# Performance work log

Hardware: AMD Instinct MI355X
Metric: run time of the kernel (lower is better)

The kernel has to match this reference:

```python
import jax, jax.numpy as jnp
import numpy as np

B, T, W, L, H, TW = 2, 4096, 2048, 2048, 8, 4
HD = L // H  # head dim for block-diagonal gate projections


def setup_inputs() -> dict:
    key = jax.random.key(0)
    ks = jax.random.split(key, 16)
    inv_sqrt_w = 1.0 / np.sqrt(W)
    inv_sqrt_l = 1.0 / np.sqrt(L)
    inv_sqrt_hd = 1.0 / np.sqrt(HD)
    return {
        "x": jax.random.normal(ks[0], (B, T, W), dtype=jnp.float32),
        "segment_pos": jnp.tile(jnp.arange(T, dtype=jnp.int32), (B, 1)),
        # linear_y, linear_x: width -> lru_width
        "w_y": jax.random.normal(ks[1], (W, L), dtype=jnp.float32) * inv_sqrt_w,
        "b_y": jnp.zeros((L,), dtype=jnp.float32),
        "w_x": jax.random.normal(ks[2], (W, L), dtype=jnp.float32) * inv_sqrt_w,
        "b_x": jnp.zeros((L,), dtype=jnp.float32),
        # linear_out: lru_width -> width
        "w_out": jax.random.normal(ks[3], (L, W), dtype=jnp.float32) * inv_sqrt_l,
        "b_out": jnp.zeros((W,), dtype=jnp.float32),
        # depthwise causal temporal conv, kernel [TW, L]
        "conv_w": jax.random.normal(ks[4], (TW, L), dtype=jnp.float32) / np.sqrt(TW),
        "conv_b": jnp.zeros((L,), dtype=jnp.float32),
        # RG-LRU: a_param and two block-diagonal gate projections
        "a_param": jax.random.uniform(ks[5], (L,), dtype=jnp.float32, minval=-2.0, maxval=1.0),
        "igate_w": jax.random.normal(ks[6], (H, HD, HD), dtype=jnp.float32) * inv_sqrt_hd,
        "igate_b": jnp.zeros((H, HD), dtype=jnp.float32),
        "agate_w": jax.random.normal(ks[7], (H, HD, HD), dtype=jnp.float32) * inv_sqrt_hd,
        "agate_b": jnp.zeros((H, HD), dtype=jnp.float32),
    }


def _block_diag_linear(u, w, b):
    # u: [B,T,L] -> [B,T,H,HD] blockwise projected -> [B,T,L]
    uh = u.reshape(u.shape[0], u.shape[1], H, HD)
    y = jnp.einsum("bthd,hde->bthe", uh, w) + b
    return y.reshape(u.shape)


def _forward(x, segment_pos, w_y, b_y, w_x, b_x, w_out, b_out,
             conv_w, conv_b, a_param, igate_w, igate_b, agate_w, agate_b):
    # gate branch: linear_y + tanh-approx GELU
    y = jax.nn.gelu(jnp.einsum("btw,wl->btl", x, w_y) + b_y, approximate=True)
    # recurrent branch: linear_x
    xb = jnp.einsum("btw,wl->btl", x, w_x) + b_x
    # causal depthwise temporal conv (width TW), zero history before t=0
    x_pad = jnp.pad(xb, ((0, 0), (TW - 1, 0), (0, 0)))
    conv = conv_b + sum(conv_w[j] * x_pad[:, j:j + T] for j in range(TW))
    # RG-LRU gates
    gate_x = jax.nn.sigmoid(_block_diag_linear(conv, igate_w, igate_b))
    gate_a = jax.nn.sigmoid(_block_diag_linear(conv, agate_w, agate_b))
    log_a = -8.0 * gate_a * jax.nn.softplus(a_param)  # [B,T,L]
    a = jnp.exp(log_a)
    reset = (segment_pos == 0)[..., None]  # [B,T,1]
    multiplier = jnp.sqrt(1.0 - jnp.exp(2.0 * log_a))
    multiplier = jnp.where(reset, 1.0, multiplier)
    normed = conv * gate_x * multiplier
    a_masked = jnp.where(reset, 0.0, a)
    # diagonal linear recurrence: h_t = a_t * h_{t-1} + normed_t
    def step(h, inp):
        a_t, x_t = inp
        h = a_t * h + x_t
        return h, h
    h0 = jnp.zeros((x.shape[0], L), dtype=x.dtype)
    _, hs = jax.lax.scan(step, h0, (a_masked.transpose(1, 0, 2), normed.transpose(1, 0, 2)))
    hs = hs.transpose(1, 0, 2)  # [B,T,L]
    # elementwise gate then output projection
    return jnp.einsum("btl,lw->btw", hs * y, w_out) + b_out


def reference(x, segment_pos, w_y, b_y, w_x, b_x, w_out, b_out,
              conv_w, conv_b, a_param, igate_w, igate_b, agate_w, agate_b):
    return _forward(x, segment_pos, w_y, b_y, w_x, b_x, w_out, b_out,
                    conv_w, conv_b, a_param, igate_w, igate_b, agate_w, agate_b)
```

## Files before the change

kernel.cpp:

```cpp
#include <hip/hip_runtime.h>
#include <cstdint>
#include <math.h>

typedef _Float16 f16;
typedef f16 f16x8 __attribute__((ext_vector_type(8)));
typedef f16 f16x4 __attribute__((ext_vector_type(4)));
typedef float f32x4 __attribute__((ext_vector_type(4)));

#define BATCH 2
#define TSEQ 4096
#define WID 2048
#define LRU 2048
#define NHEAD 8
#define HDIM 256
#define MTOT (BATCH * TSEQ)
#define CT 128
#define NC (TSEQ / CT)

__device__ __forceinline__ void gl2lds16(const f16* g, f16* l) {
  __builtin_amdgcn_global_load_lds(
      (__attribute__((address_space(1))) uint32_t*)(uintptr_t)g,
      (__attribute__((address_space(3))) uint32_t*)(uint32_t)(uintptr_t)l,
      16, 0, 0);
}

__device__ __forceinline__ float sigmoidf_(float x) { return 1.f / (1.f + expf(-x)); }
__device__ __forceinline__ float f16bits_to_f(uint32_t b) {
  return (float)__builtin_bit_cast(f16, (uint16_t)b);
}

__global__ void cast_f32_f16_kernel(const float* __restrict__ in, f16* __restrict__ out, int n4) {
  int i = blockIdx.x * 256 + threadIdx.x;
  if (i >= n4) return;
  float4 v = ((const float4*)in)[i];
  f16x4 o = { (f16)v.x, (f16)v.y, (f16)v.z, (f16)v.w };
  ((f16x4*)out)[i] = o;
}

__global__ void transpose_big_kernel(const float* __restrict__ s0, const float* __restrict__ s1,
                                     const float* __restrict__ s2, f16* __restrict__ d0,
                                     f16* __restrict__ d1, f16* __restrict__ d2) {
  __shared__ float tile[32][33];
  const int R = 2048, C = 2048;
  const float* ib = blockIdx.z == 0 ? s0 : (blockIdx.z == 1 ? s1 : s2);
  f16* ob = blockIdx.z == 0 ? d0 : (blockIdx.z == 1 ? d1 : d2);
  int c0 = blockIdx.x * 32, r0 = blockIdx.y * 32;
  int tx = threadIdx.x, ty = threadIdx.y;
#pragma unroll
  for (int i = 0; i < 32; i += 8)
    tile[ty + i][tx] = ib[(long long)(r0 + ty + i) * C + c0 + tx];
  __syncthreads();
#pragma unroll
  for (int i = 0; i < 32; i += 8)
    ob[(long long)(c0 + ty + i) * R + r0 + tx] = (f16)tile[tx][ty + i];
}

__global__ void transpose_small_kernel(const float* __restrict__ ig, const float* __restrict__ ag,
                                       f16* __restrict__ igT, f16* __restrict__ agT) {
  __shared__ float tile[32][33];
  int z = blockIdx.z;
  const float* ib = (z < 8 ? ig : ag) + (long long)(z & 7) * HDIM * HDIM;
  f16* ob = (z < 8 ? igT : agT) + (long long)(z & 7) * HDIM * HDIM;
  int c0 = blockIdx.x * 32, r0 = blockIdx.y * 32;
  int tx = threadIdx.x, ty = threadIdx.y;
#pragma unroll
  for (int i = 0; i < 32; i += 8)
    tile[ty + i][tx] = ib[(r0 + ty + i) * HDIM + c0 + tx];
  __syncthreads();
#pragma unroll
  for (int i = 0; i < 32; i += 8)
    ob[(c0 + ty + i) * HDIM + r0 + tx] = (f16)tile[tx][ty + i];
}

__global__ __launch_bounds__(256, 2) void gemm_dual(
    const f16* __restrict__ A, const f16* __restrict__ B1T, const f16* __restrict__ B2T,
    const float* __restrict__ b1, const float* __restrict__ b2,
    f16* __restrict__ Y, f16* __restrict__ X2, int M, int N, int K) {
  __shared__ __align__(16) f16 As[128 * 32];
  __shared__ __align__(16) f16 B1s[128 * 32];
  __shared__ __align__(16) f16 B2s[128 * 32];
  const int m0 = blockIdx.x * 128, n0 = blockIdx.y * 128;
  const int t = threadIdx.x;
  const int lane = t & 63, wave = t >> 6;
  const int wr = (wave >> 1) * 64, wc = (wave & 1) * 64;
  const int l15 = lane & 15, quad = lane >> 4;
  const int srow = t >> 2, scol = (t & 3) * 8;

  const f16* Ag = A + (long long)(m0 + srow) * K + scol;
  const f16* B1g = B1T + (long long)(n0 + srow) * K + scol;
  const f16* B2g = B2T + (long long)(n0 + srow) * K + scol;

  f32x4 c1[4][4] = {};
  f32x4 c2[4][4] = {};
  for (int k0 = 0; k0 < K; k0 += 32) {
    gl2lds16(Ag, &As[t * 8]);   gl2lds16(Ag + (long long)64 * K, &As[64 * 32 + t * 8]);
    gl2lds16(B1g, &B1s[t * 8]); gl2lds16(B1g + (long long)64 * K, &B1s[64 * 32 + t * 8]);
    gl2lds16(B2g, &B2s[t * 8]); gl2lds16(B2g + (long long)64 * K, &B2s[64 * 32 + t * 8]);
    Ag += 32; B1g += 32; B2g += 32;
    __syncthreads();
    f16x8 af[4], b1f[4], b2f[4];
#pragma unroll
    for (int i = 0; i < 4; ++i)
      af[i] = *(const f16x8*)&As[(wr + i * 16 + l15) * 32 + quad * 8];
#pragma unroll
    for (int j = 0; j < 4; ++j) {
      b1f[j] = *(const f16x8*)&B1s[(wc + j * 16 + l15) * 32 + quad * 8];
      b2f[j] = *(const f16x8*)&B2s[(wc + j * 16 + l15) * 32 + quad * 8];
    }
#pragma unroll
    for (int i = 0; i < 4; ++i)
#pragma unroll
      for (int j = 0; j < 4; ++j) {
        c1[i][j] = __builtin_amdgcn_mfma_f32_16x16x32_f16(af[i], b1f[j], c1[i][j], 0, 0, 0);
        c2[i][j] = __builtin_amdgcn_mfma_f32_16x16x32_f16(af[i], b2f[j], c2[i][j], 0, 0, 0);
      }
    __syncthreads();
  }
#pragma unroll
  for (int i = 0; i < 4; ++i) {
#pragma unroll
    for (int j = 0; j < 4; ++j) {
      const int col = n0 + wc + j * 16 + l15;
      const float b1v = b1[col], b2v = b2[col];
      const int row0 = m0 + wr + i * 16 + quad * 4;
#pragma unroll
      for (int r = 0; r < 4; ++r) {
        long long off = (long long)(row0 + r) * N + col;
        float v = c1[i][j][r] + b1v;
        float u = v + 0.044715f * v * v * v;
        float g = 0.5f * v * (1.f + tanhf(0.7978845608028654f * u));
        Y[off] = (f16)g;
        X2[off] = (f16)(c2[i][j][r] + b2v);
      }
    }
  }
}

__global__ __launch_bounds__(256, 2) void gemm_bt(
    const f16* __restrict__ A, const f16* __restrict__ BT, const float* __restrict__ bias,
    float* __restrict__ Cf, int M, int N, int K) {
  __shared__ __align__(16) f16 As[128 * 32];
  __shared__ __align__(16) f16 Bs[128 * 32];
  const int m0 = blockIdx.x * 128, n0 = blockIdx.y * 128;
  const int t = threadIdx.x;
  const int lane = t & 63, wave = t >> 6;
  const int wr = (wave >> 1) * 64, wc = (wave & 1) * 64;
  const int l15 = lane & 15, quad = lane >> 4;
  const int srow = t >> 2, scol = (t & 3) * 8;

  const f16* Ag = A + (long long)(m0 + srow) * K + scol;
  const f16* Bg = BT + (long long)(n0 + srow) * K + scol;

  f32x4 acc[4][4] = {};
  for (int k0 = 0; k0 < K; k0 += 32) {
    gl2lds16(Ag, &As[t * 8]); gl2lds16(Ag + (long long)64 * K, &As[64 * 32 + t * 8]);
    gl2lds16(Bg, &Bs[t * 8]); gl2lds16(Bg + (long long)64 * K, &Bs[64 * 32 + t * 8]);
    Ag += 32; Bg += 32;
    __syncthreads();
    f16x8 af[4], bf[4];
#pragma unroll
    for (int i = 0; i < 4; ++i)
      af[i] = *(const f16x8*)&As[(wr + i * 16 + l15) * 32 + quad * 8];
#pragma unroll
    for (int j = 0; j < 4; ++j)
      bf[j] = *(const f16x8*)&Bs[(wc + j * 16 + l15) * 32 + quad * 8];
#pragma unroll
    for (int i = 0; i < 4; ++i)
#pragma unroll
      for (int j = 0; j < 4; ++j)
        acc[i][j] = __builtin_amdgcn_mfma_f32_16x16x32_f16(af[i], bf[j], acc[i][j], 0, 0, 0);
    __syncthreads();
  }
#pragma unroll
  for (int i = 0; i < 4; ++i) {
#pragma unroll
    for (int j = 0; j < 4; ++j) {
      const int col = n0 + wc + j * 16 + l15;
      const float bv = bias[col];
      const int row0 = m0 + wr + i * 16 + quad * 4;
#pragma unroll
      for (int r = 0; r < 4; ++r)
        Cf[(long long)(row0 + r) * N + col] = acc[i][j][r] + bv;
    }
  }
}

__global__ __launch_bounds__(256, 2) void gates_fused(
    const f16* __restrict__ XBh, const float* __restrict__ cw, const float* __restrict__ cb,
    const f16* __restrict__ BiT, const f16* __restrict__ BaT,
    const float* __restrict__ ib, const float* __restrict__ ab,
    const float* __restrict__ a_param, const int* __restrict__ segpos,
    uint32_t* __restrict__ AN, float* __restrict__ Ac, float* __restrict__ Hc) {
  __shared__ __align__(16) f16 As[128 * 256];
  __shared__ __align__(16) f16 Bi[128 * 32];
  __shared__ __align__(16) f16 Ba[128 * 32];
  const int m0 = blockIdx.x * 128;
  const int h = blockIdx.y >> 1;
  const int half = blockIdx.y & 1;
  const int ncol0 = h * HDIM + half * 128;
  const int t = threadIdx.x;
  const int lane = t & 63, wave = t >> 6;
  const int wr = (wave >> 1) * 64, wc = (wave & 1) * 64;
  const int l15 = lane & 15, quad = lane >> 4;

#pragma unroll 4
  for (int it = 0; it < 16; ++it) {
    int idx = it * 256 + t;
    int r = idx >> 5, kc = idx & 31;
    int m = m0 + r, tpos = m & (TSEQ - 1);
    int colbase = h * HDIM + kc * 8;
    float acc[8];
    {
      float4 c0 = *(const float4*)&cb[colbase];
      float4 c1 = *(const float4*)&cb[colbase + 4];
      acc[0] = c0.x; acc[1] = c0.y; acc[2] = c0.z; acc[3] = c0.w;
      acc[4] = c1.x; acc[5] = c1.y; acc[6] = c1.z; acc[7] = c1.w;
    }
#pragma unroll
    for (int d = 0; d < 4; ++d) {
      if (tpos >= d) {
        f16x8 xv = *(const f16x8*)&XBh[(long long)(m - d) * LRU + colbase];
        float4 w0 = *(const float4*)&cw[(3 - d) * LRU + colbase];
        float4 w1 = *(const float4*)&cw[(3 - d) * LRU + colbase + 4];
        acc[0] += w0.x * (float)xv[0]; acc[1] += w0.y * (float)xv[1];
        acc[2] += w0.z * (float)xv[2]; acc[3] += w0.w * (float)xv[3];
        acc[4] += w1.x * (float)xv[4]; acc[5] += w1.y * (float)xv[5];
        acc[6] += w1.z * (float)xv[6]; acc[7] += w1.w * (float)xv[7];
      }
    }
    f16x8 o;
#pragma unroll
    for (int k = 0; k < 8; ++k) o[k] = (f16)acc[k];
    int gs = (kc & ~7) | ((kc ^ r) & 7);
    *(f16x8*)&As[r * 256 + gs * 8] = o;
  }
  __syncthreads();

  const int srow = t >> 2, scol = (t & 3) * 8;
  const f16* Big = BiT + (long long)(ncol0 + srow) * HDIM + scol;
  const f16* Bag = BaT + (long long)(ncol0 + srow) * HDIM + scol;
  f32x4 ci[4][4] = {};
  f32x4 ca[4][4] = {};
  for (int k0 = 0; k0 < HDIM; k0 += 32) {
    gl2lds16(Big, &Bi[t * 8]); gl2lds16(Big + 64 * HDIM, &Bi[64 * 32 + t * 8]);
    gl2lds16(Bag, &Ba[t * 8]); gl2lds16(Bag + 64 * HDIM, &Ba[64 * 32 + t * 8]);
    Big += 32; Bag += 32;
    __syncthreads();
    f16x8 af[4], bif[4], baf[4];
#pragma unroll
    for (int i = 0; i < 4; ++i) {
      int row = wr + i * 16 + l15;
      int g = (k0 >> 3) + quad;
      int gsw = (g & ~7) | ((g ^ row) & 7);
      af[i] = *(const f16x8*)&As[row * 256 + gsw * 8];
    }
#pragma unroll
    for (int j = 0; j < 4; ++j) {
      bif[j] = *(const f16x8*)&Bi[(wc + j * 16 + l15) * 32 + quad * 8];
      baf[j] = *(const f16x8*)&Ba[(wc + j * 16 + l15) * 32 + quad * 8];
    }
#pragma unroll
    for (int i = 0; i < 4; ++i)
#pragma unroll
      for (int j = 0; j < 4; ++j) {
        ci[i][j] = __builtin_amdgcn_mfma_f32_16x16x32_f16(af[i], bif[j], ci[i][j], 0, 0, 0);
        ca[i][j] = __builtin_amdgcn_mfma_f32_16x16x32_f16(af[i], baf[j], ca[i][j], 0, 0, 0);
      }
    __syncthreads();
  }

  const int mb = m0 >> 12;
  const int cch = (m0 & (TSEQ - 1)) >> 7;
  float Aw[4], hw[4];
#pragma unroll
  for (int j = 0; j < 4; ++j) {
    const int cl = wc + j * 16 + l15;
    const int col = ncol0 + cl;
    const float ibv = ib[col], abv = ab[col];
    const float sp = log1pf(expf(a_param[col]));
    float A4[4], h4[4];
#pragma unroll
    for (int i = 0; i < 4; ++i) {
      float Aseg = 1.f, hseg = 0.f;
#pragma unroll
      for (int r = 0; r < 4; ++r) {
        const int rowL = wr + i * 16 + quad * 4 + r;
        const int row = m0 + rowL;
        float gx = sigmoidf_(ci[i][j][r] + ibv);
        float ga = sigmoidf_(ca[i][j][r] + abv);
        float la = -8.f * ga * sp;
        bool rs = (segpos[row] == 0);
        float a = rs ? 0.f : expf(la);
        uint32_t afx = __float2uint_rn(a * 65536.f);
        if (afx > 65535u) afx = 65535u;
        float aq = (float)afx * (1.f / 65536.f);
        int cfull = half * 128 + cl;
        int g = cfull >> 3, e = cfull & 7;
        int gsw = (g & ~7) | ((g ^ rowL) & 7);
        float cv = (float)As[rowL * 256 + gsw * 8 + e];
        float mult = rs ? 1.f : sqrtf(fmaxf(1.f - aq * aq, 0.f));
        f16 nh = (f16)(cv * gx * mult);
        AN[(long long)row * LRU + col] =
            afx | ((uint32_t)__builtin_bit_cast(uint16_t, nh) << 16);
        float xq = (float)nh;
        hseg = aq * hseg + xq;
        Aseg *= aq;
      }
      A4[i] = Aseg; h4[i] = hseg;
    }
#pragma unroll
    for (int i = 0; i < 4; ++i) {
      float A = A4[i], hv = h4[i];
#pragma unroll
      for (int d = 1; d <= 2; d <<= 1) {
        int src = quad >= d ? lane - 16 * d : lane;
        float Ap = __shfl(A, src);
        float hp = __shfl(hv, src);
        if (quad >= d) { hv = A * hp + hv; A = Ap * A; }
      }
      A4[i] = __shfl(A, 48 + l15);
      h4[i] = __shfl(hv, 48 + l15);
    }
    float Awv = 1.f, hwv = 0.f;
#pragma unroll
    for (int i = 0; i < 4; ++i) { hwv = A4[i] * hwv + h4[i]; Awv *= A4[i]; }
    Aw[j] = Awv; hw[j] = hwv;
  }
  float* carry = (float*)Bi;
  __syncthreads();
  if (wr == 0 && quad == 0) {
#pragma unroll
    for (int j = 0; j < 4; ++j) {
      int cl = wc + j * 16 + l15;
      carry[cl * 2] = Aw[j]; carry[cl * 2 + 1] = hw[j];
    }
  }
  __syncthreads();
  if (wr == 64 && quad == 0) {
#pragma unroll
    for (int j = 0; j < 4; ++j) {
      int cl = wc + j * 16 + l15;
      float At = carry[cl * 2], ht = carry[cl * 2 + 1];
      float A = At * Aw[j];
      float hv = Aw[j] * ht + hw[j];
      int o = (mb * NC + cch) * LRU + ncol0 + cl;
      Ac[o] = A; Hc[o] = hv;
    }
  }
}

__global__ void scan2_kernel(const float* __restrict__ Ac, const float* __restrict__ Hc,
                             float* __restrict__ P) {
  int l = blockIdx.x * 256 + threadIdx.x;
  int b = blockIdx.y;
  float hv = 0.f;
#pragma unroll 8
  for (int c = 0; c < NC; ++c) {
    int o = (b * NC + c) * LRU + l;
    P[o] = hv;
    hv = Ac[o] * hv + Hc[o];
  }
}

__global__ void scan3_kernel(const uint32_t* __restrict__ AN,
                             const float* __restrict__ P, const f16* __restrict__ Yh,
                             f16* __restrict__ G) {
  int l = blockIdx.x * 256 + threadIdx.x;
  int c = blockIdx.y, b = blockIdx.z;
  long long base = ((long long)b * TSEQ + (long long)c * CT) * LRU + l;
  float hv = P[(b * NC + c) * LRU + l];
#pragma unroll 4
  for (int s = 0; s < CT; ++s) {
    long long o = base + (long long)s * LRU;
    uint32_t p = AN[o];
    float a = (float)(p & 0xFFFFu) * (1.f / 65536.f);
    float x = f16bits_to_f(p >> 16);
    hv = a * hv + x;
    G[o] = (f16)(hv * (float)Yh[o]);
  }
}

extern "C" void kernel_launch(void* const* d_in, const int* in_sizes, int n_in,
                              void* d_out, int out_size, void* d_ws, size_t ws_size,
                              hipStream_t stream) {
  (void)in_sizes; (void)n_in; (void)out_size; (void)ws_size;
  const float* x          = (const float*)d_in[0];
  const int*   segment_pos= (const int*)d_in[1];
  const float* w_y        = (const float*)d_in[2];
  const float* b_y        = (const float*)d_in[3];
  const float* w_x        = (const float*)d_in[4];
  const float* b_x        = (const float*)d_in[5];
  const float* w_out      = (const float*)d_in[6];
  const float* b_out      = (const float*)d_in[7];
  const float* conv_w     = (const float*)d_in[8];
  const float* conv_b     = (const float*)d_in[9];
  const float* a_param    = (const float*)d_in[10];
  const float* igate_w    = (const float*)d_in[11];
  const float* igate_b    = (const float*)d_in[12];
  const float* agate_w    = (const float*)d_in[13];
  const float* agate_b    = (const float*)d_in[14];
  float* out = (float*)d_out;

  char* base = (char*)d_ws;
  size_t off = 0;
  auto alloc = [&](size_t nbytes) -> void* {
    void* p = base + off;
    off = (off + nbytes + 255) & ~(size_t)255;
    return p;
  };
  f16*     Xh    = (f16*)alloc((size_t)MTOT * LRU * 2);
  f16*     Yh    = (f16*)alloc((size_t)MTOT * LRU * 2);
  f16*     XBh   = (f16*)alloc((size_t)MTOT * LRU * 2);
  uint32_t* AN   = (uint32_t*)alloc((size_t)MTOT * LRU * 4);
  f16*     wyT   = (f16*)alloc((size_t)WID * LRU * 2);
  f16*     wxT   = (f16*)alloc((size_t)WID * LRU * 2);
  f16*     woutT = (f16*)alloc((size_t)LRU * WID * 2);
  f16*     igwT  = (f16*)alloc((size_t)NHEAD * HDIM * HDIM * 2);
  f16*     agwT  = (f16*)alloc((size_t)NHEAD * HDIM * HDIM * 2);
  float*   Ac    = (float*)alloc((size_t)BATCH * NC * LRU * 4);
  float*   Hc    = (float*)alloc((size_t)BATCH * NC * LRU * 4);
  float*   Pc    = (float*)alloc((size_t)BATCH * NC * LRU * 4);
  f16*     G     = Xh;

  dim3 tb32(32, 8);
  cast_f32_f16_kernel<<<(MTOT * LRU / 4 + 255) / 256, 256, 0, stream>>>(x, Xh, MTOT * LRU / 4);
  transpose_big_kernel<<<dim3(64, 64, 3), tb32, 0, stream>>>(w_y, w_x, w_out, wyT, wxT, woutT);
  transpose_small_kernel<<<dim3(8, 8, 16), tb32, 0, stream>>>(igate_w, agate_w, igwT, agwT);
  gemm_dual<<<dim3(MTOT / 128, LRU / 128), 256, 0, stream>>>(
      Xh, wyT, wxT, b_y, b_x, Yh, XBh, MTOT, LRU, WID);
  gates_fused<<<dim3(MTOT / 128, 2 * NHEAD), 256, 0, stream>>>(
      XBh, conv_w, conv_b, igwT, agwT, igate_b, agate_b, a_param, segment_pos, AN, Ac, Hc);
  scan2_kernel<<<dim3(LRU / 256, BATCH), 256, 0, stream>>>(Ac, Hc, Pc);
  scan3_kernel<<<dim3(LRU / 256, NC, BATCH), 256, 0, stream>>>(AN, Pc, Yh, G);
  gemm_bt<<<dim3(MTOT / 128, WID / 128), 256, 0, stream>>>(G, woutT, b_out, out, MTOT, WID, LRU);
}
```

Measured before the change: 573.2 us.

## Fuse chunked scan into gates kernel with decoupled look-back carry chain

Replaces the gates kernel plus two separate scan kernels with a single kernel that computes the full within-tile scan in registers. Carries pass between sequential chunks through global flags and atomics, with block order set by a ticket counter, so the packed AN intermediate (a 32-bit value per element written and re-read) is no longer needed. The conv stage now reuses a register window of XBh rows instead of reloading four rows per output, and the cast/transpose prep kernels are merged into one launch. In exchange, chunks along time are serialized through spin-waits on flags.

```diff
diff --git a/kernel.cpp b/kernel.cpp
--- a/kernel.cpp
+++ b/kernel.cpp
@@ -14,8 +14,8 @@
 #define NHEAD 8
 #define HDIM 256
 #define MTOT (BATCH * TSEQ)
-#define CT 128
-#define NC (TSEQ / CT)
+#define NCHUNK 32
+#define NMT 64
 
 __device__ __forceinline__ void gl2lds16(const f16* g, f16* l) {
   __builtin_amdgcn_global_load_lds(
@@ -25,27 +25,39 @@
 }
 
 __device__ __forceinline__ float sigmoidf_(float x) { return 1.f / (1.f + expf(-x)); }
-__device__ __forceinline__ float f16bits_to_f(uint32_t b) {
-  return (float)__builtin_bit_cast(f16, (uint16_t)b);
-}
-
-__global__ void cast_f32_f16_kernel(const float* __restrict__ in, f16* __restrict__ out, int n4) {
-  int i = blockIdx.x * 256 + threadIdx.x;
-  if (i >= n4) return;
-  float4 v = ((const float4*)in)[i];
-  f16x4 o = { (f16)v.x, (f16)v.y, (f16)v.z, (f16)v.w };
-  ((f16x4*)out)[i] = o;
-}
-
-__global__ void transpose_big_kernel(const float* __restrict__ s0, const float* __restrict__ s1,
-                                     const float* __restrict__ s2, f16* __restrict__ d0,
-                                     f16* __restrict__ d1, f16* __restrict__ d2) {
+
+__global__ void prep_kernel(const float* __restrict__ x, f16* __restrict__ Xh,
+                            const float* __restrict__ w_y, const float* __restrict__ w_x,
+                            const float* __restrict__ w_out,
+                            f16* __restrict__ wyT, f16* __restrict__ wxT, f16* __restrict__ woutT,
+                            const float* __restrict__ ig, const float* __restrict__ ag,
+                            f16* __restrict__ igT, f16* __restrict__ agT) {
   __shared__ float tile[32][33];
-  const int R = 2048, C = 2048;
-  const float* ib = blockIdx.z == 0 ? s0 : (blockIdx.z == 1 ? s1 : s2);
-  f16* ob = blockIdx.z == 0 ? d0 : (blockIdx.z == 1 ? d1 : d2);
-  int c0 = blockIdx.x * 32, r0 = blockIdx.y * 32;
-  int tx = threadIdx.x, ty = threadIdx.y;
+  const int bid = blockIdx.x, t = threadIdx.x;
+  if (bid < 16384) {
+    int i = bid * 256 + t;
+    float4 v = ((const float4*)x)[i];
+    f16x4 o = { (f16)v.x, (f16)v.y, (f16)v.z, (f16)v.w };
+    ((f16x4*)Xh)[i] = o;
+    return;
+  }
+  const int tx = t & 31, ty = t >> 5;
+  const float* ib; f16* ob; int R, C, c0, r0;
+  if (bid < 28672) {
+    int idx = bid - 16384;
+    int z = idx >> 12, tl = idx & 4095;
+    ib = z == 0 ? w_y : (z == 1 ? w_x : w_out);
+    ob = z == 0 ? wyT : (z == 1 ? wxT : woutT);
+    R = 2048; C = 2048;
+    c0 = (tl & 63) * 32; r0 = (tl >> 6) * 32;
+  } else {
+    int idx = bid - 28672;
+    int z = idx >> 6, tl = idx & 63;
+    ib = (z < 8 ? ig : ag) + (long long)(z & 7) * HDIM * HDIM;
+    ob = (z < 8 ? igT : agT) + (long long)(z & 7) * HDIM * HDIM;
+    R = HDIM; C = HDIM;
+    c0 = (tl & 7) * 32; r0 = (tl >> 3) * 32;
+  }
 #pragma unroll
   for (int i = 0; i < 32; i += 8)
     tile[ty + i][tx] = ib[(long long)(r0 + ty + i) * C + c0 + tx];
@@ -53,23 +65,6 @@
 #pragma unroll
   for (int i = 0; i < 32; i += 8)
     ob[(long long)(c0 + ty + i) * R + r0 + tx] = (f16)tile[tx][ty + i];
-}
-
-__global__ void transpose_small_kernel(const float* __restrict__ ig, const float* __restrict__ ag,
-                                       f16* __restrict__ igT, f16* __restrict__ agT) {
-  __shared__ float tile[32][33];
-  int z = blockIdx.z;
-  const float* ib = (z < 8 ? ig : ag) + (long long)(z & 7) * HDIM * HDIM;
-  f16* ob = (z < 8 ? igT : agT) + (long long)(z & 7) * HDIM * HDIM;
-  int c0 = blockIdx.x * 32, r0 = blockIdx.y * 32;
-  int tx = threadIdx.x, ty = threadIdx.y;
-#pragma unroll
-  for (int i = 0; i < 32; i += 8)
-    tile[ty + i][tx] = ib[(r0 + ty + i) * HDIM + c0 + tx];
-  __syncthreads();
-#pragma unroll
-  for (int i = 0; i < 32; i += 8)
-    ob[(c0 + ty + i) * HDIM + r0 + tx] = (f16)tile[tx][ty + i];
 }
 
 __global__ __launch_bounds__(256, 2) void gemm_dual(
@@ -185,54 +180,75 @@
   }
 }
 
-__global__ __launch_bounds__(256, 2) void gates_fused(
+__global__ __launch_bounds__(256, 2) void gates_scan(
     const f16* __restrict__ XBh, const float* __restrict__ cw, const float* __restrict__ cb,
     const f16* __restrict__ BiT, const f16* __restrict__ BaT,
     const float* __restrict__ ib, const float* __restrict__ ab,
     const float* __restrict__ a_param, const int* __restrict__ segpos,
-    uint32_t* __restrict__ AN, float* __restrict__ Ac, float* __restrict__ Hc) {
+    const f16* __restrict__ Yh, f16* __restrict__ G,
+    int* __restrict__ ticket, int* __restrict__ Flags, float* __restrict__ Carry) {
   __shared__ __align__(16) f16 As[128 * 256];
   __shared__ __align__(16) f16 Bi[128 * 32];
   __shared__ __align__(16) f16 Ba[128 * 32];
-  const int m0 = blockIdx.x * 128;
-  const int h = blockIdx.y >> 1;
-  const int half = blockIdx.y & 1;
-  const int ncol0 = h * HDIM + half * 128;
   const int t = threadIdx.x;
   const int lane = t & 63, wave = t >> 6;
   const int wr = (wave >> 1) * 64, wc = (wave & 1) * 64;
   const int l15 = lane & 15, quad = lane >> 4;
 
-#pragma unroll 4
-  for (int it = 0; it < 16; ++it) {
+  if (t == 0) ((int*)Bi)[0] = atomicAdd(ticket, 1);
+  __syncthreads();
+  const int v = ((int*)Bi)[0];
+  const int bz = v & 1, cg = (v >> 1) & 15, chunk = v >> 5;
+  const int mt = bz * NCHUNK + chunk;
+  const int m0 = mt * 128;
+  const int h = cg >> 1, half = cg & 1;
+  const int ncol0 = h * HDIM + half * 128;
+  const int mtcg = mt * 16 + cg;
+
+#pragma unroll
+  for (int it = 0; it < 2; ++it) {
     int idx = it * 256 + t;
-    int r = idx >> 5, kc = idx & 31;
-    int m = m0 + r, tpos = m & (TSEQ - 1);
+    int kc = idx & 31;
+    int r0 = (idx >> 5) * 8;
     int colbase = h * HDIM + kc * 8;
-    float acc[8];
-    {
-      float4 c0 = *(const float4*)&cb[colbase];
-      float4 c1 = *(const float4*)&cb[colbase + 4];
-      acc[0] = c0.x; acc[1] = c0.y; acc[2] = c0.z; acc[3] = c0.w;
-      acc[4] = c1.x; acc[5] = c1.y; acc[6] = c1.z; acc[7] = c1.w;
-    }
-#pragma unroll
-    for (int d = 0; d < 4; ++d) {
-      if (tpos >= d) {
-        f16x8 xv = *(const f16x8*)&XBh[(long long)(m - d) * LRU + colbase];
-        float4 w0 = *(const float4*)&cw[(3 - d) * LRU + colbase];
-        float4 w1 = *(const float4*)&cw[(3 - d) * LRU + colbase + 4];
-        acc[0] += w0.x * (float)xv[0]; acc[1] += w0.y * (float)xv[1];
-        acc[2] += w0.z * (float)xv[2]; acc[3] += w0.w * (float)xv[3];
-        acc[4] += w1.x * (float)xv[4]; acc[5] += w1.y * (float)xv[5];
-        acc[6] += w1.z * (float)xv[6]; acc[7] += w1.w * (float)xv[7];
-      }
-    }
-    f16x8 o;
-#pragma unroll
-    for (int k = 0; k < 8; ++k) o[k] = (f16)acc[k];
-    int gs = (kc & ~7) | ((kc ^ r) & 7);
-    *(f16x8*)&As[r * 256 + gs * 8] = o;
+    f16x8 gr[11];
+#pragma unroll
+    for (int gi = 0; gi < 11; ++gi) {
+      f16x8 g = {};
+      int m = m0 + r0 - 3 + gi;
+      if (m >= 0) g = *(const f16x8*)&XBh[(long long)m * LRU + colbase];
+      gr[gi] = g;
+    }
+    float4 cb0 = *(const float4*)&cb[colbase];
+    float4 cb1 = *(const float4*)&cb[colbase + 4];
+    float4 w0[4], w1[4];
+#pragma unroll
+    for (int dd = 0; dd < 4; ++dd) {
+      w0[dd] = *(const float4*)&cw[dd * LRU + colbase];
+      w1[dd] = *(const float4*)&cw[dd * LRU + colbase + 4];
+    }
+#pragma unroll
+    for (int r = 0; r < 8; ++r) {
+      int rr = r0 + r;
+      int m = m0 + rr, tpos = m & (TSEQ - 1);
+      float acc[8] = {cb0.x, cb0.y, cb0.z, cb0.w, cb1.x, cb1.y, cb1.z, cb1.w};
+#pragma unroll
+      for (int d = 0; d < 4; ++d) {
+        if (tpos >= d) {
+          f16x8 xv = gr[3 + r - d];
+          float4 a0 = w0[3 - d], a1 = w1[3 - d];
+          acc[0] += a0.x * (float)xv[0]; acc[1] += a0.y * (float)xv[1];
+          acc[2] += a0.z * (float)xv[2]; acc[3] += a0.w * (float)xv[3];
+          acc[4] += a1.x * (float)xv[4]; acc[5] += a1.y * (float)xv[5];
+          acc[6] += a1.z * (float)xv[6]; acc[7] += a1.w * (float)xv[7];
+        }
+      }
+      f16x8 o;
+#pragma unroll
+      for (int k = 0; k < 8; ++k) o[k] = (f16)acc[k];
+      int gs = (kc & ~7) | ((kc ^ rr) & 7);
+      *(f16x8*)&As[rr * 256 + gs * 8] = o;
+    }
   }
   __syncthreads();
 
@@ -269,8 +285,6 @@
     __syncthreads();
   }
 
-  const int mb = m0 >> 12;
-  const int cch = (m0 & (TSEQ - 1)) >> 7;
   float Aw[4], hw[4];
 #pragma unroll
   for (int j = 0; j < 4; ++j) {
@@ -278,10 +292,10 @@
     const int col = ncol0 + cl;
     const float ibv = ib[col], abv = ab[col];
     const float sp = log1pf(expf(a_param[col]));
-    float A4[4], h4[4];
+    float A_E = 1.f, h_E = 0.f;
 #pragma unroll
     for (int i = 0; i < 4; ++i) {
-      float Aseg = 1.f, hseg = 0.f;
+      float Aacc = 1.f, hacc = 0.f;
 #pragma unroll
       for (int r = 0; r < 4; ++r) {
         const int rowL = wr + i * 16 + quad * 4 + r;
@@ -291,92 +305,114 @@
         float la = -8.f * ga * sp;
         bool rs = (segpos[row] == 0);
         float a = rs ? 0.f : expf(la);
-        uint32_t afx = __float2uint_rn(a * 65536.f);
-        if (afx > 65535u) afx = 65535u;
-        float aq = (float)afx * (1.f / 65536.f);
+        float mult = rs ? 1.f : sqrtf(fmaxf(1.f - a * a, 0.f));
         int cfull = half * 128 + cl;
         int g = cfull >> 3, e = cfull & 7;
         int gsw = (g & ~7) | ((g ^ rowL) & 7);
         float cv = (float)As[rowL * 256 + gsw * 8 + e];
-        float mult = rs ? 1.f : sqrtf(fmaxf(1.f - aq * aq, 0.f));
-        f16 nh = (f16)(cv * gx * mult);
-        AN[(long long)row * LRU + col] =
-            afx | ((uint32_t)__builtin_bit_cast(uint16_t, nh) << 16);
-        float xq = (float)nh;
-        hseg = aq * hseg + xq;
-        Aseg *= aq;
-      }
-      A4[i] = Aseg; h4[i] = hseg;
-    }
+        float xv = cv * gx * mult;
+        hacc = a * hacc + xv;
+        Aacc = a * Aacc;
+        ci[i][j][r] = hacc;
+        ca[i][j][r] = Aacc;
+      }
+      float A1 = Aacc, h1 = hacc;
+      {
+        int src = lane >= 16 ? lane - 16 : lane;
+        float Ap = __shfl(A1, src), hp = __shfl(h1, src);
+        if (quad >= 1) { h1 = A1 * hp + h1; A1 = A1 * Ap; }
+        src = lane >= 32 ? lane - 32 : lane;
+        Ap = __shfl(A1, src); hp = __shfl(h1, src);
+        if (quad >= 2) { h1 = A1 * hp + h1; A1 = A1 * Ap; }
+      }
+      int srcx = lane >= 16 ? lane - 16 : lane;
+      float Ae = __shfl(A1, srcx), he = __shfl(h1, srcx);
+      if (quad == 0) { Ae = 1.f; he = 0.f; }
+      float A_p = Ae * A_E;
+      float h_p = Ae * h_E + he;
+#pragma unroll
+      for (int r = 0; r < 4; ++r) {
+        float Ael = ca[i][j][r], hel = ci[i][j][r];
+        ci[i][j][r] = Ael * h_p + hel;
+        ca[i][j][r] = A_p * Ael;
+      }
+      float At3 = __shfl(A1, 48 + l15), ht3 = __shfl(h1, 48 + l15);
+      h_E = At3 * h_E + ht3;
+      A_E = At3 * A_E;
+    }
+    Aw[j] = A_E; hw[j] = h_E;
+  }
+
+  float2* carryW = (float2*)Ba;
+  float* Pl = (float*)((char*)Ba + 4096);
+  if (wr == 0 && quad == 0) {
+#pragma unroll
+    for (int j = 0; j < 4; ++j) {
+      float2 cwv; cwv.x = Aw[j]; cwv.y = hw[j];
+      carryW[wc + j * 16 + l15] = cwv;
+    }
+  }
+  __syncthreads();
+  float A_tot[4], h_tot[4];
+  if (wr == 64) {
+#pragma unroll
+    for (int j = 0; j < 4; ++j) {
+      float2 bb = carryW[wc + j * 16 + l15];
+#pragma unroll
+      for (int i = 0; i < 4; ++i)
+#pragma unroll
+        for (int r = 0; r < 4; ++r) {
+          float Ael = ca[i][j][r];
+          ci[i][j][r] = Ael * bb.y + ci[i][j][r];
+          ca[i][j][r] = bb.x * Ael;
+        }
+      A_tot[j] = Aw[j] * bb.x;
+      h_tot[j] = Aw[j] * bb.y + hw[j];
+    }
+  }
+
+  if (chunk > 0) {
+    if (t < 128) {
+      const int* fl = &Flags[mtcg - 16];
+      while (__hip_atomic_load(fl, __ATOMIC_ACQUIRE, __HIP_MEMORY_SCOPE_AGENT) == 0)
+        __builtin_amdgcn_s_sleep(8);
+      Pl[t] = __hip_atomic_load(&Carry[(long long)(mtcg - 16) * 128 + t],
+                                __ATOMIC_RELAXED, __HIP_MEMORY_SCOPE_AGENT);
+    }
+  } else if (t < 128) {
+    Pl[t] = 0.f;
+  }
+  __syncthreads();
+
+  if (wr == 64 && quad == 0) {
+#pragma unroll
+    for (int j = 0; j < 4; ++j) {
+      int cl = wc + j * 16 + l15;
+      float hend = A_tot[j] * Pl[cl] + h_tot[j];
+      __hip_atomic_store(&Carry[(long long)mtcg * 128 + cl], hend,
+                         __ATOMIC_RELAXED, __HIP_MEMORY_SCOPE_AGENT);
+    }
+  }
+  __threadfence();
+  __syncthreads();
+  if (t == 0)
+    __hip_atomic_store(&Flags[mtcg], 1, __ATOMIC_RELEASE, __HIP_MEMORY_SCOPE_AGENT);
+
+#pragma unroll
+  for (int j = 0; j < 4; ++j) {
+    const int cl = wc + j * 16 + l15;
+    const int col = ncol0 + cl;
+    const float P = Pl[cl];
 #pragma unroll
     for (int i = 0; i < 4; ++i) {
-      float A = A4[i], hv = h4[i];
-#pragma unroll
-      for (int d = 1; d <= 2; d <<= 1) {
-        int src = quad >= d ? lane - 16 * d : lane;
-        float Ap = __shfl(A, src);
-        float hp = __shfl(hv, src);
-        if (quad >= d) { hv = A * hp + hv; A = Ap * A; }
-      }
-      A4[i] = __shfl(A, 48 + l15);
-      h4[i] = __shfl(hv, 48 + l15);
-    }
-    float Awv = 1.f, hwv = 0.f;
-#pragma unroll
-    for (int i = 0; i < 4; ++i) { hwv = A4[i] * hwv + h4[i]; Awv *= A4[i]; }
-    Aw[j] = Awv; hw[j] = hwv;
-  }
-  float* carry = (float*)Bi;
-  __syncthreads();
-  if (wr == 0 && quad == 0) {
-#pragma unroll
-    for (int j = 0; j < 4; ++j) {
-      int cl = wc + j * 16 + l15;
-      carry[cl * 2] = Aw[j]; carry[cl * 2 + 1] = hw[j];
-    }
-  }
-  __syncthreads();
-  if (wr == 64 && quad == 0) {
-#pragma unroll
-    for (int j = 0; j < 4; ++j) {
-      int cl = wc + j * 16 + l15;
-      float At = carry[cl * 2], ht = carry[cl * 2 + 1];
-      float A = At * Aw[j];
-      float hv = Aw[j] * ht + hw[j];
-      int o = (mb * NC + cch) * LRU + ncol0 + cl;
-      Ac[o] = A; Hc[o] = hv;
-    }
-  }
-}
-
-__global__ void scan2_kernel(const float* __restrict__ Ac, const float* __restrict__ Hc,
-                             float* __restrict__ P) {
-  int l = blockIdx.x * 256 + threadIdx.x;
-  int b = blockIdx.y;
-  float hv = 0.f;
-#pragma unroll 8
-  for (int c = 0; c < NC; ++c) {
-    int o = (b * NC + c) * LRU + l;
-    P[o] = hv;
-    hv = Ac[o] * hv + Hc[o];
-  }
-}
-
-__global__ void scan3_kernel(const uint32_t* __restrict__ AN,
-                             const float* __restrict__ P, const f16* __restrict__ Yh,
-                             f16* __restrict__ G) {
-  int l = blockIdx.x * 256 + threadIdx.x;
-  int c = blockIdx.y, b = blockIdx.z;
-  long long base = ((long long)b * TSEQ + (long long)c * CT) * LRU + l;
-  float hv = P[(b * NC + c) * LRU + l];
-#pragma unroll 4
-  for (int s = 0; s < CT; ++s) {
-    long long o = base + (long long)s * LRU;
-    uint32_t p = AN[o];
-    float a = (float)(p & 0xFFFFu) * (1.f / 65536.f);
-    float x = f16bits_to_f(p >> 16);
-    hv = a * hv + x;
-    G[o] = (f16)(hv * (float)Yh[o]);
+#pragma unroll
+      for (int r = 0; r < 4; ++r) {
+        const int row = m0 + wr + i * 16 + quad * 4 + r;
+        float hg = ca[i][j][r] * P + ci[i][j][r];
+        long long off = (long long)row * LRU + col;
+        G[off] = (f16)(hg * (float)Yh[off]);
+      }
+    }
   }
 }
 
@@ -408,29 +444,26 @@
     off = (off + nbytes + 255) & ~(size_t)255;
     return p;
   };
-  f16*     Xh    = (f16*)alloc((size_t)MTOT * LRU * 2);
-  f16*     Yh    = (f16*)alloc((size_t)MTOT * LRU * 2);
-  f16*     XBh   = (f16*)alloc((size_t)MTOT * LRU * 2);
-  uint32_t* AN   = (uint32_t*)alloc((size_t)MTOT * LRU * 4);
-  f16*     wyT   = (f16*)alloc((size_t)WID * LRU * 2);
-  f16*     wxT   = (f16*)alloc((size_t)WID * LRU * 2);
-  f16*     woutT = (f16*)alloc((size_t)LRU * WID * 2);
-  f16*     igwT  = (f16*)alloc((size_t)NHEAD * HDIM * HDIM * 2);
-  f16*     agwT  = (f16*)alloc((size_t)NHEAD * HDIM * HDIM * 2);
-  float*   Ac    = (float*)alloc((size_t)BATCH * NC * LRU * 4);
-  float*   Hc    = (float*)alloc((size_t)BATCH * NC * LRU * 4);
-  float*   Pc    = (float*)alloc((size_t)BATCH * NC * LRU * 4);
-  f16*     G     = Xh;
-
-  dim3 tb32(32, 8);
-  cast_f32_f16_kernel<<<(MTOT * LRU / 4 + 255) / 256, 256, 0, stream>>>(x, Xh, MTOT * LRU / 4);
-  transpose_big_kernel<<<dim3(64, 64, 3), tb32, 0, stream>>>(w_y, w_x, w_out, wyT, wxT, woutT);
-  transpose_small_kernel<<<dim3(8, 8, 16), tb32, 0, stream>>>(igate_w, agate_w, igwT, agwT);
+  f16*   Xh    = (f16*)alloc((size_t)MTOT * LRU * 2);
+  f16*   Yh    = (f16*)alloc((size_t)MTOT * LRU * 2);
+  f16*   XBh   = (f16*)alloc((size_t)MTOT * LRU * 2);
+  f16*   wyT   = (f16*)alloc((size_t)WID * LRU * 2);
+  f16*   wxT   = (f16*)alloc((size_t)WID * LRU * 2);
+  f16*   woutT = (f16*)alloc((size_t)LRU * WID * 2);
+  f16*   igwT  = (f16*)alloc((size_t)NHEAD * HDIM * HDIM * 2);
+  f16*   agwT  = (f16*)alloc((size_t)NHEAD * HDIM * HDIM * 2);
+  float* Carry = (float*)alloc((size_t)NMT * 16 * 128 * 4);
+  int*   Flags = (int*)alloc((size_t)NMT * 16 * 4 + 256);
+  int*   ticket= Flags + NMT * 16;
+  f16*   G     = Xh;
+
+  hipMemsetAsync(Flags, 0, (size_t)NMT * 16 * 4 + 4, stream);
+  prep_kernel<<<29696, 256, 0, stream>>>(x, Xh, w_y, w_x, w_out, wyT, wxT, woutT,
+                                         igate_w, agate_w, igwT, agwT);
   gemm_dual<<<dim3(MTOT / 128, LRU / 128), 256, 0, stream>>>(
       Xh, wyT, wxT, b_y, b_x, Yh, XBh, MTOT, LRU, WID);
-  gates_fused<<<dim3(MTOT / 128, 2 * NHEAD), 256, 0, stream>>>(
-      XBh, conv_w, conv_b, igwT, agwT, igate_b, agate_b, a_param, segment_pos, AN, Ac, Hc);
-  scan2_kernel<<<dim3(LRU / 256, BATCH), 256, 0, stream>>>(Ac, Hc, Pc);
-  scan3_kernel<<<dim3(LRU / 256, NC, BATCH), 256, 0, stream>>>(AN, Pc, Yh, G);
+  gates_scan<<<BATCH * 16 * NCHUNK, 256, 0, stream>>>(
+      XBh, conv_w, conv_b, igwT, agwT, igate_b, agate_b, a_param, segment_pos,
+      Yh, G, ticket, Flags, Carry);
   gemm_bt<<<dim3(MTOT / 128, WID / 128), 256, 0, stream>>>(G, woutT, b_out, out, MTOT, WID, LRU);
 }
```

Measured after the change: 1.332 ms. 2.32x slower.
